# Performance work log

Hardware: AMD Instinct MI355X
Metric: run time of the kernel (lower is better)

Reference implementation:

```python
import jax, jax.numpy as jnp
import numpy as np

NUM_ENT = 100000
NUM_REL = 50
NUM_EDGES = 200000
NNZ = 1000000
D = 128
BATCH = 4096
C = 1.0  # curvature k of the Lorentz manifold


def lorentz_linear(x, W, b, scale_param):
    # HyboNet-style LorentzLinear: linear map, then rescale so output lies on hyperboloid
    x = x @ W.T + b                                   # [N, D]
    time = jax.nn.sigmoid(x[..., :1]) * jnp.exp(scale_param) + 1.1   # [N, 1]
    xs = x[..., 1:]
    sqnorm = jnp.clip(jnp.sum(xs * xs, axis=-1, keepdims=True), 1e-8, None)
    s = jnp.sqrt((time * time - 1.0) / sqnorm)
    return jnp.concatenate([time, xs * s], axis=-1)


def logmap0(x, k):
    # Lorentz log map at the origin: time component -> 0, spatial rescaled by arccosh distance
    sqrtK = jnp.sqrt(jnp.asarray(k, x.dtype))
    y = x[..., 1:]
    y_norm = jnp.clip(jnp.linalg.norm(y, axis=-1, keepdims=True), 1e-8, None)
    theta = jnp.clip(x[..., :1] / sqrtK, 1.0 + 1e-7, None)
    spatial = sqrtK * jnp.arccosh(theta) * y / y_norm
    return jnp.concatenate([jnp.zeros_like(x[..., :1]), spatial], axis=-1)


def h2conv(X, emb_ty, vertex, edges, ty, lin_W, lin_b, lin_scale, eps):
    N = X.shape[0]
    Xl = lorentz_linear(X, lin_W, lin_b, lin_scale)           # [N, D]
    Xve = Xl[vertex] - emb_ty[ty]                             # [nnz, D] gather - relation translation
    Xe = jax.ops.segment_sum(Xve, edges, num_segments=NUM_EDGES)  # [E, D]
    Xev = Xe[edges]                                           # [nnz, D]
    Xv = jax.ops.segment_sum(Xev, vertex, num_segments=N)     # [N, D]
    return eps * Xv + Xl


def setup_inputs():
    key = jax.random.key(0)
    ks = jax.random.split(key, 20)
    n_ty = (NUM_REL - 1) * 6
    return {
        "emb_E": jax.random.normal(ks[0], (NUM_ENT, D), jnp.float32),
        "emb_R": jax.random.normal(ks[1], (NUM_REL, D), jnp.float32),
        "emb_ty": jax.random.normal(ks[2], (n_ty, D), jnp.float32),
        "lin_W": jax.random.normal(ks[3], (D, D), jnp.float32) * (1.0 / np.sqrt(D)),
        "lin_b": jnp.zeros((D,), jnp.float32),
        "lin_scale": jnp.asarray(np.log(10.0), jnp.float32),
        "eps": jnp.asarray([0.5], jnp.float32),
        "ms": jax.random.uniform(ks[4], (BATCH, 6), dtype=jnp.float32),
        "r_idx": jax.random.randint(ks[5], (BATCH,), 0, NUM_REL),
        "e1_idx": jax.random.randint(ks[6], (BATCH,), 0, NUM_ENT),
        "e2_idx": jax.random.randint(ks[7], (BATCH,), 0, NUM_ENT),
        "e3_idx": jax.random.randint(ks[8], (BATCH,), 0, NUM_ENT),
        "e4_idx": jax.random.randint(ks[9], (BATCH,), 0, NUM_ENT),
        "e5_idx": jax.random.randint(ks[10], (BATCH,), 0, NUM_ENT),
        "e6_idx": jax.random.randint(ks[11], (BATCH,), 0, NUM_ENT),
        "vertex": jax.random.randint(ks[12], (NNZ,), 0, NUM_ENT),
        "edges": jax.random.randint(ks[13], (NNZ,), 0, NUM_EDGES),
        "ty": jax.random.randint(ks[14], (NNZ,), 0, n_ty),
        "bs": BATCH,
    }


def reference(emb_E, emb_R, emb_ty, lin_W, lin_b, lin_scale, eps, ms,
              r_idx, e1_idx, e2_idx, e3_idx, e4_idx, e5_idx, e6_idx,
              vertex, edges, ty, bs):
    # (expmap0 result in the torch code is immediately overwritten, so omitted)
    E_e = h2conv(emb_E, emb_ty, vertex, edges, ty, lin_W, lin_b, lin_scale, eps)
    E_e = logmap0(E_e, C)
    E_e = E_e.at[0].set(1.0)
    R_e = emb_R.at[0].set(1.0)
    r = R_e[r_idx]
    x = (E_e[e1_idx] * E_e[e2_idx] * E_e[e3_idx] *
         E_e[e4_idx] * E_e[e5_idx] * E_e[e6_idx] * r)   # [B, D]
    return jnp.sum(x, axis=1)
```

## Files before the change

### kernel.cpp

```cpp
#include <hip/hip_runtime.h>
#include <math.h>

#define NUM_ENT   100000
#define NUM_REL   50
#define NUM_EDGES 200000
#define NNZ       1000000
#define DIM       128
#define BATCH     4096

#define CAP_E 32
#define CAP_V 40

#define XL_OFF  0
#define XH_OFF  (NUM_ENT * DIM)
#define XE_ROWS 150000
#define XE_OFF  (XH_OFF + NUM_ENT * DIM / 2)
#define INT_OFF (XE_OFF + XE_ROWS * DIM)

#define CUR_E   0
#define CUR_V   (CUR_E + NUM_EDGES)
#define BMV_O   (CUR_V + NUM_ENT)
#define FLAGE_O (BMV_O + 3136)
#define NV_CNT  (FLAGE_O + 50000)
#define NE_CNT  (NV_CNT + 1)
#define ZERO_N  (NE_CNT + 1)
#define VLIST   (ZERO_N)
#define ELIST   (VLIST + 24704)
#define EINV    (ELIST + NUM_EDGES)
#define PAYE    (EINV + NUM_EDGES)
#define PAYV    (PAYE + NUM_EDGES * CAP_E)
#define WSPHI   (PAYV + NUM_ENT * CAP_V)
#define WSPLO   (WSPHI + 8192)

#define FILL8_BLOCKS  489
#define ELIST4_BLOCKS 196

typedef __attribute__((ext_vector_type(8))) short sh8;
typedef __attribute__((ext_vector_type(4))) short sh4;
typedef __attribute__((ext_vector_type(4))) float f32x4;
typedef __attribute__((ext_vector_type(4))) _Float16 h4f;

__device__ __forceinline__ int bmtest(const unsigned* __restrict__ bm, int v) {
    return (bm[v >> 5] >> (v & 31)) & 1u;
}

__device__ __forceinline__ void split1(float x, unsigned short& h, unsigned short& l) {
    __bf16 hb = (__bf16)x;
    float hf = (float)hb;
    __bf16 lb = (__bf16)(x - hf);
    h = __builtin_bit_cast(unsigned short, hb);
    l = __builtin_bit_cast(unsigned short, lb);
}

__global__ __launch_bounds__(256, 4) void k_gemm_lorentz(const float* __restrict__ X,
                                                         const unsigned short* __restrict__ WhiG,
                                                         const unsigned short* __restrict__ WloG,
                                                         const float* __restrict__ bias,
                                                         const float* __restrict__ scale_p,
                                                         float* __restrict__ Y,
                                                         _Float16* __restrict__ Yh,
                                                         const unsigned* __restrict__ bmv) {
    __shared__ unsigned short Ahi[64 * 40], Alo[64 * 40];
    __shared__ unsigned short Bhi[128 * 40], Blo[128 * 40];
    __shared__ float biasS[128];

    const int t = threadIdx.x;
    const int row0 = blockIdx.x * 64;
    const int lane = t & 63, wv = t >> 6;
    const int cq = lane & 15, qd = lane >> 4;
    const float4* X4 = (const float4*)X;

    if (t < 128) biasS[t] = bias[t];

    f32x4 acc[8];
#pragma unroll
    for (int tn = 0; tn < 8; ++tn) acc[tn] = (f32x4){0.f, 0.f, 0.f, 0.f};

    for (int kc = 0; kc < 4; ++kc) {
#pragma unroll
        for (int i = 0; i < 2; ++i) {
            int q = t + 256 * i;
            int row = q >> 3, k4 = q & 7;
            int gr = row0 + row;
            float4 xv = make_float4(0.f, 0.f, 0.f, 0.f);
            if (gr < NUM_ENT) xv = X4[gr * 32 + kc * 8 + k4];
            unsigned short h0, h1, h2, h3, l0, l1, l2, l3;
            split1(xv.x, h0, l0); split1(xv.y, h1, l1);
            split1(xv.z, h2, l2); split1(xv.w, h3, l3);
            *(sh4*)&Ahi[row * 40 + k4 * 4] = (sh4){(short)h0, (short)h1, (short)h2, (short)h3};
            *(sh4*)&Alo[row * 40 + k4 * 4] = (sh4){(short)l0, (short)l1, (short)l2, (short)l3};
        }
#pragma unroll
        for (int i = 0; i < 4; ++i) {
            int q = t + 256 * i;
            int wr = q >> 3, k4 = q & 7;
            *(sh4*)&Bhi[wr * 40 + k4 * 4] =
                *(const sh4*)&WhiG[wr * 128 + kc * 32 + k4 * 4];
            *(sh4*)&Blo[wr * 40 + k4 * 4] =
                *(const sh4*)&WloG[wr * 128 + kc * 32 + k4 * 4];
        }
        __syncthreads();

        sh8 ah = *(const sh8*)&Ahi[(wv * 16 + cq) * 40 + qd * 8];
        sh8 al = *(const sh8*)&Alo[(wv * 16 + cq) * 40 + qd * 8];
#pragma unroll
        for (int tn = 0; tn < 8; ++tn) {
            sh8 bh = *(const sh8*)&Bhi[(tn * 16 + cq) * 40 + qd * 8];
            sh8 bl = *(const sh8*)&Blo[(tn * 16 + cq) * 40 + qd * 8];
            acc[tn] = __builtin_amdgcn_mfma_f32_16x16x32_bf16(ah, bh, acc[tn], 0, 0, 0);
            acc[tn] = __builtin_amdgcn_mfma_f32_16x16x32_bf16(ah, bl, acc[tn], 0, 0, 0);
            acc[tn] = __builtin_amdgcn_mfma_f32_16x16x32_bf16(al, bh, acc[tn], 0, 0, 0);
        }
        __syncthreads();
    }

    float es = expf(scale_p[0]);
    float psum[4] = {0.f, 0.f, 0.f, 0.f};
#pragma unroll
    for (int tn = 0; tn < 8; ++tn) {
        float bj = biasS[tn * 16 + cq];
#pragma unroll
        for (int reg = 0; reg < 4; ++reg) {
            float y = acc[tn][reg] + bj;
            acc[tn][reg] = y;
            psum[reg] += y * y;
        }
    }
#pragma unroll
    for (int off = 1; off < 16; off <<= 1) {
#pragma unroll
        for (int reg = 0; reg < 4; ++reg)
            psum[reg] += __shfl_xor(psum[reg], off, 64);
    }
    float srow[4], trow[4];
#pragma unroll
    for (int reg = 0; reg < 4; ++reg) {
        float y0 = __shfl(acc[0][reg], lane & 48, 64);
        float time = es / (1.f + expf(-y0)) + 1.1f;
        float ps = fmaxf(psum[reg] - y0 * y0, 1e-8f);
        srow[reg] = sqrtf((time * time - 1.f) / ps);
        trow[reg] = time;
    }
    int growv[4], fl[4];
#pragma unroll
    for (int reg = 0; reg < 4; ++reg) {
        int grow = row0 + wv * 16 + qd * 4 + reg;
        growv[reg] = grow;
        fl[reg] = (grow < NUM_ENT) ? bmtest(bmv, grow) : 0;
    }
#pragma unroll
    for (int tn = 0; tn < 8; ++tn) {
        int col = tn * 16 + cq;
#pragma unroll
        for (int reg = 0; reg < 4; ++reg) {
            if (growv[reg] < NUM_ENT) {
                float y = acc[tn][reg];
                float val = (col == 0) ? trow[reg] : y * srow[reg];
                Yh[growv[reg] * 128 + col] = (_Float16)val;
                if (fl[reg]) Y[growv[reg] * 128 + col] = val;
            }
        }
    }
}

__global__ __launch_bounds__(256) void k_flagv(const int* __restrict__ e1,
                                               const int* __restrict__ e2,
                                               const int* __restrict__ e3,
                                               const int* __restrict__ e4,
                                               const int* __restrict__ e5,
                                               const int* __restrict__ e6,
                                               unsigned* __restrict__ bmv,
                                               int* __restrict__ vlist,
                                               int* __restrict__ nv,
                                               const float* __restrict__ W,
                                               unsigned short* __restrict__ Whi,
                                               unsigned short* __restrict__ Wlo) {
    if (blockIdx.x >= 16) {
        int i = (blockIdx.x - 16) * 256 + threadIdx.x;
        unsigned short h, l;
        split1(W[i], h, l);
        Whi[i] = h; Wlo[i] = l;
        return;
    }
    int i = blockIdx.x * 256 + threadIdx.x;
    if (i >= BATCH) return;
    int idx[6] = {e1[i], e2[i], e3[i], e4[i], e5[i], e6[i]};
#pragma unroll
    for (int k = 0; k < 6; ++k) {
        int v = idx[k];
        unsigned bit = 1u << (v & 31);
        unsigned old = atomicOr(&bmv[v >> 5], bit);
        if (!(old & bit))
            vlist[atomicAdd(nv, 1)] = v;
    }
}

__global__ __launch_bounds__(256) void k_flage(const int* __restrict__ edges,
                                               const int* __restrict__ vertex,
                                               const unsigned* __restrict__ bmv,
                                               unsigned char* __restrict__ flag_e) {
    int i4 = (blockIdx.x * 256 + threadIdx.x) * 4;
    if (i4 + 3 < NNZ) {
        int4 v = *(const int4*)&vertex[i4];
        int4 e = *(const int4*)&edges[i4];
        if (bmtest(bmv, v.x)) flag_e[e.x] = 1;
        if (bmtest(bmv, v.y)) flag_e[e.y] = 1;
        if (bmtest(bmv, v.z)) flag_e[e.z] = 1;
        if (bmtest(bmv, v.w)) flag_e[e.w] = 1;
    } else {
        for (int i = i4; i < NNZ; ++i)
            if (bmtest(bmv, vertex[i])) flag_e[edges[i]] = 1;
    }
}

__global__ __launch_bounds__(256) void k_fill(const int* __restrict__ edges,
                                              const int* __restrict__ vertex,
                                              const int* __restrict__ tyi,
                                              const unsigned char* __restrict__ flag_e,
                                              const unsigned* __restrict__ bmv,
                                              int* __restrict__ cur_e,
                                              int* __restrict__ cur_v,
                                              int* __restrict__ pay_e,
                                              int* __restrict__ pay_v,
                                              int* __restrict__ elist,
                                              int* __restrict__ einv,
                                              int* __restrict__ ne) {
    int bid = blockIdx.x;
    if (bid >= FILL8_BLOCKS) {
        int i4 = ((bid - FILL8_BLOCKS) * 256 + threadIdx.x) * 4;
        if (i4 >= NUM_EDGES) return;
        int f[4], cnt = 0;
#pragma unroll
        for (int k = 0; k < 4; ++k) {
            int i = i4 + k;
            f[k] = (i < NUM_EDGES) ? flag_e[i] : 0;
            cnt += f[k];
        }
        if (cnt) {
            int g = atomicAdd(ne, cnt);
#pragma unroll
            for (int k = 0; k < 4; ++k) {
                if (f[k]) {
                    elist[g] = i4 + k;
                    einv[i4 + k] = g;
                    ++g;
                }
            }
        }
        return;
    }
    int i8 = (bid * 256 + threadIdx.x) * 8;
    if (i8 >= NNZ) return;
    int vv[8], ee[8], tt[8], nit;
    if (i8 + 7 < NNZ) {
        int4 v0 = *(const int4*)&vertex[i8];
        int4 v1 = *(const int4*)&vertex[i8 + 4];
        int4 e0 = *(const int4*)&edges[i8];
        int4 e1 = *(const int4*)&edges[i8 + 4];
        int4 t0 = *(const int4*)&tyi[i8];
        int4 t1 = *(const int4*)&tyi[i8 + 4];
        vv[0] = v0.x; vv[1] = v0.y; vv[2] = v0.z; vv[3] = v0.w;
        vv[4] = v1.x; vv[5] = v1.y; vv[6] = v1.z; vv[7] = v1.w;
        ee[0] = e0.x; ee[1] = e0.y; ee[2] = e0.z; ee[3] = e0.w;
        ee[4] = e1.x; ee[5] = e1.y; ee[6] = e1.z; ee[7] = e1.w;
        tt[0] = t0.x; tt[1] = t0.y; tt[2] = t0.z; tt[3] = t0.w;
        tt[4] = t1.x; tt[5] = t1.y; tt[6] = t1.z; tt[7] = t1.w;
        nit = 8;
    } else {
        nit = NNZ - i8;
        for (int k = 0; k < nit; ++k) {
            vv[k] = vertex[i8 + k]; ee[k] = edges[i8 + k]; tt[k] = tyi[i8 + k];
        }
    }
#pragma unroll 8
    for (int k = 0; k < nit; ++k) {
        int v = vv[k], e = ee[k];
        if (flag_e[e]) {
            int p = atomicAdd(&cur_e[e], 1);
            if (p < CAP_E) pay_e[e * CAP_E + p] = (v << 9) | tt[k];
        }
        if (bmtest(bmv, v)) {
            int q = atomicAdd(&cur_v[v], 1);
            if (q < CAP_V) pay_v[v * CAP_V + q] = e;
        }
    }
}

__global__ __launch_bounds__(256) void k_gatherE(const _Float16* __restrict__ Xlh,
                                                 const float* __restrict__ Ty,
                                                 const int* __restrict__ elist,
                                                 const int* __restrict__ ne_p,
                                                 const int* __restrict__ cur_e,
                                                 const int* __restrict__ pay_e,
                                                 float* __restrict__ Xe) {
    int tid = blockIdx.x * 256 + threadIdx.x;
    int g = tid >> 5, l = tid & 31;
    if (g >= ne_p[0] || g >= XE_ROWS) return;
    int e = elist[g];
    int n = cur_e[e]; n = (n > CAP_E) ? CAP_E : n;
    int myPay = pay_e[e * CAP_E + l];
    const int base = threadIdx.x & 32;
    const h4f* Xh4 = (const h4f*)Xlh;
    const float4* Ty4 = (const float4*)Ty;
    float4 acc = make_float4(0.f, 0.f, 0.f, 0.f);
    int k = 0;
    for (; k + 4 <= n; k += 4) {
        int pe0 = __shfl(myPay, base + k,     64);
        int pe1 = __shfl(myPay, base + k + 1, 64);
        int pe2 = __shfl(myPay, base + k + 2, 64);
        int pe3 = __shfl(myPay, base + k + 3, 64);
        h4f a0 = Xh4[(pe0 >> 9) * 32 + l];
        h4f a1 = Xh4[(pe1 >> 9) * 32 + l];
        h4f a2 = Xh4[(pe2 >> 9) * 32 + l];
        h4f a3 = Xh4[(pe3 >> 9) * 32 + l];
        float4 c0 = Ty4[(pe0 & 511) * 32 + l];
        float4 c1 = Ty4[(pe1 & 511) * 32 + l];
        float4 c2 = Ty4[(pe2 & 511) * 32 + l];
        float4 c3 = Ty4[(pe3 & 511) * 32 + l];
        acc.x += (float)a0.x - c0.x; acc.y += (float)a0.y - c0.y;
        acc.z += (float)a0.z - c0.z; acc.w += (float)a0.w - c0.w;
        acc.x += (float)a1.x - c1.x; acc.y += (float)a1.y - c1.y;
        acc.z += (float)a1.z - c1.z; acc.w += (float)a1.w - c1.w;
        acc.x += (float)a2.x - c2.x; acc.y += (float)a2.y - c2.y;
        acc.z += (float)a2.z - c2.z; acc.w += (float)a2.w - c2.w;
        acc.x += (float)a3.x - c3.x; acc.y += (float)a3.y - c3.y;
        acc.z += (float)a3.z - c3.z; acc.w += (float)a3.w - c3.w;
    }
    for (; k < n; ++k) {
        int pe = __shfl(myPay, base + k, 64);
        int v = pe >> 9, tt = pe & 511;
        h4f a = Xh4[v * 32 + l];
        float4 c = Ty4[tt * 32 + l];
        acc.x += (float)a.x - c.x; acc.y += (float)a.y - c.y;
        acc.z += (float)a.z - c.z; acc.w += (float)a.w - c.w;
    }
    ((float4*)Xe)[g * 32 + l] = acc;
}

__global__ __launch_bounds__(256) void k_gatherV_final(float* __restrict__ XlEe,
                                                       const float* __restrict__ Xe,
                                                       const int* __restrict__ cur_v,
                                                       const int* __restrict__ pay_v,
                                                       const int* __restrict__ einv,
                                                       const int* __restrict__ vlist,
                                                       const int* __restrict__ nv_p,
                                                       const float* __restrict__ eps_p) {
    int gid = blockIdx.x * 256 + threadIdx.x;
    int idx = gid >> 6, lane = gid & 63;
    if (idx >= nv_p[0]) return;
    int w = vlist[idx];
    int n = cur_v[w]; n = (n > CAP_V) ? CAP_V : n;
    int pidx = (lane < CAP_V) ? lane : (CAP_V - 1);
    int myE = pay_v[w * CAP_V + pidx];
    myE = (pidx < n) ? myE : 0;
    int myG = einv[myE];
    float sa = 0.f, sb = 0.f;
    int k = 0;
    for (; k + 4 <= n; k += 4) {
        int g0 = __shfl(myG, k,     64);
        int g1 = __shfl(myG, k + 1, 64);
        int g2 = __shfl(myG, k + 2, 64);
        int g3 = __shfl(myG, k + 3, 64);
        float a0 = Xe[g0 * 128 + lane],      a1 = Xe[g1 * 128 + lane];
        float a2 = Xe[g2 * 128 + lane],      a3 = Xe[g3 * 128 + lane];
        float b0 = Xe[g0 * 128 + 64 + lane], b1 = Xe[g1 * 128 + 64 + lane];
        float b2 = Xe[g2 * 128 + 64 + lane], b3 = Xe[g3 * 128 + 64 + lane];
        sa += a0 + a1 + a2 + a3;
        sb += b0 + b1 + b2 + b3;
    }
    for (; k < n; ++k) {
        int g = __shfl(myG, k, 64);
        sa += Xe[g * 128 + lane];
        sb += Xe[g * 128 + 64 + lane];
    }
    float eps = eps_p[0];
    float xa = fmaf(eps, sa, XlEe[w * 128 + lane]);
    float xb = fmaf(eps, sb, XlEe[w * 128 + 64 + lane]);
    float x0 = __shfl(xa, 0, 64);
    float sq = xa * xa + xb * xb;
#pragma unroll
    for (int off = 32; off > 0; off >>= 1) sq += __shfl_xor(sq, off, 64);
    sq = fmaxf(sq - x0 * x0, 0.f);
    float ynorm = fmaxf(sqrtf(sq), 1e-8f);
    float theta = fmaxf(x0, 1.f + 1e-7f);
    float fac = logf(theta + sqrtf(theta * theta - 1.f)) / ynorm;
    float oa = (lane == 0) ? 0.f : xa * fac;
    float ob = xb * fac;
    if (w == 0) { oa = 1.f; ob = 1.f; }
    XlEe[w * 128 + lane]      = oa;
    XlEe[w * 128 + 64 + lane] = ob;
}

__global__ __launch_bounds__(256) void k_out(const float* __restrict__ Ee,
                                             const float* __restrict__ R,
                                             const int* __restrict__ r_idx,
                                             const int* __restrict__ e1,
                                             const int* __restrict__ e2,
                                             const int* __restrict__ e3,
                                             const int* __restrict__ e4,
                                             const int* __restrict__ e5,
                                             const int* __restrict__ e6,
                                             float* __restrict__ out) {
    int gid = blockIdx.x * 256 + threadIdx.x;
    int b = gid >> 6, lane = gid & 63;
    if (b >= BATCH) return;
    int i1 = e1[b], i2 = e2[b], i3 = e3[b], i4 = e4[b], i5 = e5[b], i6 = e6[b];
    int rr = r_idx[b];
    float pa = Ee[i1 * 128 + lane] * Ee[i2 * 128 + lane] * Ee[i3 * 128 + lane]
             * Ee[i4 * 128 + lane] * Ee[i5 * 128 + lane] * Ee[i6 * 128 + lane];
    float pb = Ee[i1 * 128 + 64 + lane] * Ee[i2 * 128 + 64 + lane] * Ee[i3 * 128 + 64 + lane]
             * Ee[i4 * 128 + 64 + lane] * Ee[i5 * 128 + 64 + lane] * Ee[i6 * 128 + 64 + lane];
    float ra = (rr == 0) ? 1.f : R[rr * 128 + lane];
    float rb = (rr == 0) ? 1.f : R[rr * 128 + 64 + lane];
    float s = pa * ra + pb * rb;
#pragma unroll
    for (int off = 32; off > 0; off >>= 1) s += __shfl_xor(s, off, 64);
    if (lane == 0) out[b] = s;
}

extern "C" void kernel_launch(void* const* d_in, const int* in_sizes, int n_in,
                              void* d_out, int out_size, void* d_ws, size_t ws_size,
                              hipStream_t stream) {
    const float* emb_E     = (const float*)d_in[0];
    const float* emb_R     = (const float*)d_in[1];
    const float* emb_ty    = (const float*)d_in[2];
    const float* lin_W     = (const float*)d_in[3];
    const float* lin_b     = (const float*)d_in[4];
    const float* lin_scale = (const float*)d_in[5];
    const float* eps       = (const float*)d_in[6];
    const int* r_idx  = (const int*)d_in[8];
    const int* e1     = (const int*)d_in[9];
    const int* e2     = (const int*)d_in[10];
    const int* e3     = (const int*)d_in[11];
    const int* e4     = (const int*)d_in[12];
    const int* e5     = (const int*)d_in[13];
    const int* e6     = (const int*)d_in[14];
    const int* vertex = (const int*)d_in[15];
    const int* edges  = (const int*)d_in[16];
    const int* tyi    = (const int*)d_in[17];

    float* ws = (float*)d_ws;
    float* Xl = ws + XL_OFF;
    _Float16* Xlh = (_Float16*)(ws + XH_OFF);
    float* Xe = ws + XE_OFF;
    int*   ib = (int*)(ws + INT_OFF);
    int* cur_e  = ib + CUR_E;
    int* cur_v  = ib + CUR_V;
    unsigned* bmv = (unsigned*)(ib + BMV_O);
    unsigned char* flag_e = (unsigned char*)(ib + FLAGE_O);
    int* nv     = ib + NV_CNT;
    int* ne     = ib + NE_CNT;
    int* vlist  = ib + VLIST;
    int* elist  = ib + ELIST;
    int* einv   = ib + EINV;
    int* pay_e  = ib + PAYE;
    int* pay_v  = ib + PAYV;
    unsigned short* Whi = (unsigned short*)(ib + WSPHI);
    unsigned short* Wlo = (unsigned short*)(ib + WSPLO);

    hipMemsetAsync(cur_e, 0, (size_t)ZERO_N * sizeof(int), stream);

    k_flagv<<<16 + 64, 256, 0, stream>>>(e1, e2, e3, e4, e5, e6,
                                         bmv, vlist, nv,
                                         lin_W, Whi, Wlo);
    k_flage<<<(NNZ / 4 + 255) / 256, 256, 0, stream>>>(edges, vertex, bmv, flag_e);
    k_fill<<<FILL8_BLOCKS + ELIST4_BLOCKS, 256, 0, stream>>>(edges, vertex, tyi,
                                                             flag_e, bmv,
                                                             cur_e, cur_v,
                                                             pay_e, pay_v,
                                                             elist, einv, ne);

    k_gemm_lorentz<<<(NUM_ENT + 63) / 64, 256, 0, stream>>>(emb_E, Whi, Wlo, lin_b,
                                                            lin_scale, Xl, Xlh,
                                                            bmv);
    k_gatherE<<<(NUM_EDGES * 32) / 256, 256, 0, stream>>>(Xlh, emb_ty, elist, ne,
                                                          cur_e, pay_e, Xe);
    k_gatherV_final<<<(BATCH * 6 * 64) / 256, 256, 0, stream>>>(Xl, Xe, cur_v,
                                                                pay_v, einv,
                                                                vlist, nv, eps);
    k_out<<<(BATCH * 64) / 256, 256, 0, stream>>>(Xl, emb_R, r_idx,
                                                  e1, e2, e3, e4, e5, e6,
                                                  (float*)d_out);
}
```

Before: 299.3 us.

## Fuse edge-flag pass into the Lorentz GEMM kernel via interleaved block roles

Merges the edge-flagging scan into the GEMM launch: every fourth block does the flag scan over eight nnz entries per thread, and the other three blocks compute GEMM tiles. The GEMM is also moved ahead of k_fill, so both independent jobs run concurrently in one launch instead of as two serialized kernels. In gatherV_final, the base row load is hoisted before the accumulation loop so its latency overlaps with the gathers. The risks are GEMM blocks landing unevenly across CUs and the GEMM tile mapping (grp*3+sub) needing to cover all tiles correctly.

```diff
diff --git a/kernel.cpp b/kernel.cpp
--- a/kernel.cpp
+++ b/kernel.cpp
@@ -34,6 +34,9 @@
 
 #define FILL8_BLOCKS  489
 #define ELIST4_BLOCKS 196
+#define FLAGE8_BLOCKS 489
+#define GEMM_TILES    1563
+#define GF_GRID       2084
 
 typedef __attribute__((ext_vector_type(8))) short sh8;
 typedef __attribute__((ext_vector_type(4))) short sh4;
@@ -52,20 +55,46 @@
     l = __builtin_bit_cast(unsigned short, lb);
 }
 
-__global__ __launch_bounds__(256, 4) void k_gemm_lorentz(const float* __restrict__ X,
-                                                         const unsigned short* __restrict__ WhiG,
-                                                         const unsigned short* __restrict__ WloG,
-                                                         const float* __restrict__ bias,
-                                                         const float* __restrict__ scale_p,
-                                                         float* __restrict__ Y,
-                                                         _Float16* __restrict__ Yh,
-                                                         const unsigned* __restrict__ bmv) {
+__global__ __launch_bounds__(256, 4) void k_gemm_flage(const float* __restrict__ X,
+                                                       const unsigned short* __restrict__ WhiG,
+                                                       const unsigned short* __restrict__ WloG,
+                                                       const float* __restrict__ bias,
+                                                       const float* __restrict__ scale_p,
+                                                       float* __restrict__ Y,
+                                                       _Float16* __restrict__ Yh,
+                                                       const unsigned* __restrict__ bmv,
+                                                       const int* __restrict__ edges,
+                                                       const int* __restrict__ vertex,
+                                                       unsigned char* __restrict__ flag_e) {
+    const int bid = blockIdx.x;
+    const int sub = bid & 3, grp = bid >> 2;
+    const int t = threadIdx.x;
+
+    if (sub == 3) {
+        if (grp >= FLAGE8_BLOCKS) return;
+        int i8 = (grp * 256 + t) * 8;
+        if (i8 >= NNZ) return;
+        int4 v0 = *(const int4*)&vertex[i8];
+        int4 v1 = *(const int4*)&vertex[i8 + 4];
+        int4 e0 = *(const int4*)&edges[i8];
+        int4 e1 = *(const int4*)&edges[i8 + 4];
+        if (bmtest(bmv, v0.x)) flag_e[e0.x] = 1;
+        if (bmtest(bmv, v0.y)) flag_e[e0.y] = 1;
+        if (bmtest(bmv, v0.z)) flag_e[e0.z] = 1;
+        if (bmtest(bmv, v0.w)) flag_e[e0.w] = 1;
+        if (bmtest(bmv, v1.x)) flag_e[e1.x] = 1;
+        if (bmtest(bmv, v1.y)) flag_e[e1.y] = 1;
+        if (bmtest(bmv, v1.z)) flag_e[e1.z] = 1;
+        if (bmtest(bmv, v1.w)) flag_e[e1.w] = 1;
+        return;
+    }
+
     __shared__ unsigned short Ahi[64 * 40], Alo[64 * 40];
     __shared__ unsigned short Bhi[128 * 40], Blo[128 * 40];
     __shared__ float biasS[128];
 
-    const int t = threadIdx.x;
-    const int row0 = blockIdx.x * 64;
+    const int tile = grp * 3 + sub;
+    const int row0 = tile * 64;
     const int lane = t & 63, wv = t >> 6;
     const int cq = lane & 15, qd = lane >> 4;
     const float4* X4 = (const float4*)X;
@@ -192,24 +221,6 @@
         unsigned old = atomicOr(&bmv[v >> 5], bit);
         if (!(old & bit))
             vlist[atomicAdd(nv, 1)] = v;
-    }
-}
-
-__global__ __launch_bounds__(256) void k_flage(const int* __restrict__ edges,
-                                               const int* __restrict__ vertex,
-                                               const unsigned* __restrict__ bmv,
-                                               unsigned char* __restrict__ flag_e) {
-    int i4 = (blockIdx.x * 256 + threadIdx.x) * 4;
-    if (i4 + 3 < NNZ) {
-        int4 v = *(const int4*)&vertex[i4];
-        int4 e = *(const int4*)&edges[i4];
-        if (bmtest(bmv, v.x)) flag_e[e.x] = 1;
-        if (bmtest(bmv, v.y)) flag_e[e.y] = 1;
-        if (bmtest(bmv, v.z)) flag_e[e.z] = 1;
-        if (bmtest(bmv, v.w)) flag_e[e.w] = 1;
-    } else {
-        for (int i = i4; i < NNZ; ++i)
-            if (bmtest(bmv, vertex[i])) flag_e[edges[i]] = 1;
     }
 }
 
@@ -354,6 +365,8 @@
     int myE = pay_v[w * CAP_V + pidx];
     myE = (pidx < n) ? myE : 0;
     int myG = einv[myE];
+    float base_a = XlEe[w * 128 + lane];
+    float base_b = XlEe[w * 128 + 64 + lane];
     float sa = 0.f, sb = 0.f;
     int k = 0;
     for (; k + 4 <= n; k += 4) {
@@ -374,8 +387,8 @@
         sb += Xe[g * 128 + 64 + lane];
     }
     float eps = eps_p[0];
-    float xa = fmaf(eps, sa, XlEe[w * 128 + lane]);
-    float xb = fmaf(eps, sb, XlEe[w * 128 + 64 + lane]);
+    float xa = fmaf(eps, sa, base_a);
+    float xb = fmaf(eps, sb, base_b);
     float x0 = __shfl(xa, 0, 64);
     float sq = xa * xa + xb * xb;
 #pragma unroll
@@ -463,16 +476,17 @@
     k_flagv<<<16 + 64, 256, 0, stream>>>(e1, e2, e3, e4, e5, e6,
                                          bmv, vlist, nv,
                                          lin_W, Whi, Wlo);
-    k_flage<<<(NNZ / 4 + 255) / 256, 256, 0, stream>>>(edges, vertex, bmv, flag_e);
+
+    k_gemm_flage<<<GF_GRID, 256, 0, stream>>>(emb_E, Whi, Wlo, lin_b,
+                                              lin_scale, Xl, Xlh, bmv,
+                                              edges, vertex, flag_e);
+
     k_fill<<<FILL8_BLOCKS + ELIST4_BLOCKS, 256, 0, stream>>>(edges, vertex, tyi,
                                                              flag_e, bmv,
                                                              cur_e, cur_v,
                                                              pay_e, pay_v,
                                                              elist, einv, ne);
 
-    k_gemm_lorentz<<<(NUM_ENT + 63) / 64, 256, 0, stream>>>(emb_E, Whi, Wlo, lin_b,
-                                                            lin_scale, Xl, Xlh,
-                                                            bmv);
     k_gatherE<<<(NUM_EDGES * 32) / 256, 256, 0, stream>>>(Xlh, emb_ty, elist, ne,
                                                           cur_e, pay_e, Xe);
     k_gatherV_final<<<(BATCH * 6 * 64) / 256, 256, 0, stream>>>(Xl, Xe, cur_v,
```

Measured after the change: 306.0 us. 1.02x slower.
